# Optimization experiments

Measured on AMD Instinct MI355X. Metric: run time of the kernel, lower is better.

The kernel has to match this reference:

```python
import jax, jax.numpy as jnp
import numpy as np

HEAD_SIZE = 8
MODEL_SIZE = 512
K_SIZE = 64
V_SIZE = 64
B, L = 4, 2048


def setup_inputs() -> dict:
    key = jax.random.key(0)
    ks = jax.random.split(key, 12)
    s = 0.02
    inp = {
        "q": jax.random.normal(ks[0], (B, L, MODEL_SIZE), jnp.float32),
        "k": jax.random.normal(ks[1], (B, L, MODEL_SIZE), jnp.float32),
        "v": jax.random.normal(ks[2], (B, L, MODEL_SIZE), jnp.float32),
        "attn_mask": jax.random.randint(ks[3], (B, L, L), 0, 2).astype(jnp.bool_),
        "Wq": jax.random.normal(ks[4], (K_SIZE, MODEL_SIZE), jnp.float32) * s,
        "bq": jnp.zeros((K_SIZE,), jnp.float32),
        "Wk": jax.random.normal(ks[5], (K_SIZE, MODEL_SIZE), jnp.float32) * s,
        "bk": jnp.zeros((K_SIZE,), jnp.float32),
        "Wv": jax.random.normal(ks[6], (V_SIZE, MODEL_SIZE), jnp.float32) * s,
        "bv": jnp.zeros((V_SIZE,), jnp.float32),
        "Wp": jax.random.normal(ks[7], (MODEL_SIZE, HEAD_SIZE * V_SIZE), jnp.float32) * s,
        "bp": jnp.zeros((MODEL_SIZE,), jnp.float32),
    }
    return inp


def reference(q, k, v, attn_mask, Wq, bq, Wk, bk, Wv, bv, Wp, bp):
    # Original module applies the same linear_q/k/v to head-repeated tensors,
    # so every head is identical; compute once and tile (exactly equal math).
    temperature = jnp.asarray(MODEL_SIZE, q.dtype) ** 0.5  # note: sqrt(model_size), not sqrt(k_size)
    qp = jnp.einsum('bld,kd->blk', q, Wq) + bq  # (B, Lq, k_size)
    kp = jnp.einsum('bld,kd->blk', k, Wk) + bk  # (B, Lk, k_size)
    vp = jnp.einsum('bld,kd->blk', v, Wv) + bv  # (B, Lk, v_size)
    attn = jnp.einsum('bqd,bkd->bqk', qp, kp) / temperature  # (B, Lq, Lk)
    attn = jnp.where(attn_mask, -jnp.inf, attn)
    attn = jax.nn.softmax(attn, axis=-1)  # dropout is identity at eval
    out = jnp.einsum('bqk,bkd->bqd', attn, vp)  # (B, Lq, v_size)
    out = jnp.tile(out, (1, 1, HEAD_SIZE))  # concat of identical per-head outputs
    out = jnp.einsum('blh,mh->blm', out, Wp) + bp  # (B, Lq, model_size)
    return out
```

## Files before the change

kernel.cpp:

```cpp
#include <hip/hip_runtime.h>

#define B_ 4
#define L_ 2048
#define MD_ 512
#define KV_ 64
#define NKT_ (L_ / 64)
#define KSPLIT 16
#define NT_ 2

typedef unsigned short u16;
typedef unsigned char u8;
typedef unsigned int u32;
typedef unsigned long long u64;
typedef __attribute__((ext_vector_type(8))) short bf16x8;
typedef __attribute__((ext_vector_type(4))) float f32x4;
typedef __attribute__((ext_vector_type(4))) u32 u32x4;
typedef __attribute__((ext_vector_type(4))) u16 u16x4;

#define INV_T 0.044194173824159216f

static __device__ __forceinline__ u16 f2bf(float x) {
  u32 u = __float_as_uint(x);
  return (u16)((u + 0x7FFFu + ((u >> 16) & 1u)) >> 16);
}
static __device__ __forceinline__ float bf2f(u16 u) {
  return __uint_as_float((u32)u << 16);
}
static __device__ __forceinline__ f32x4 zero4() {
  f32x4 z = {0.f, 0.f, 0.f, 0.f};
  return z;
}
static __device__ __forceinline__ f32x4 mfma16(bf16x8 a, bf16x8 b, f32x4 c) {
  return __builtin_amdgcn_mfma_f32_16x16x32_bf16(a, b, c, 0, 0, 0);
}

__global__ __launch_bounds__(256) void mha_prep(
    const float* __restrict__ Wq, const float* __restrict__ Wk,
    const float* __restrict__ Wv, const float* __restrict__ bq,
    const float* __restrict__ bk, const float* __restrict__ bv,
    const float* __restrict__ Wp, u16* __restrict__ WtT,
    float* __restrict__ bqkv, u16* __restrict__ WpT) {
  int t = blockIdx.x * 256 + threadIdx.x;
  if (t < 3 * 64 * 512) {
    int p = t >> 15, c = (t >> 9) & 63, d = t & 511;
    const float* W = (p == 0) ? Wq : ((p == 1) ? Wk : Wv);
    WtT[(p * 64 + c) * 520 + d] = f2bf(W[c * 512 + d]);
  } else if (t < 3 * 64 * 512 + 512 * 64) {
    int i = t - 3 * 64 * 512;
    int m = i >> 6, d = i & 63;
    float s = 0.f;
#pragma unroll
    for (int h = 0; h < 8; h++) s += Wp[m * 512 + h * 64 + d];
    WpT[m * 72 + d] = f2bf(s);
  } else if (t < 3 * 64 * 512 + 512 * 64 + 192) {
    int j = t - (3 * 64 * 512 + 512 * 64);
    int p = j >> 6;
    const float* bb = (p == 0) ? bq : ((p == 1) ? bk : bv);
    bqkv[j] = bb[j & 63];
  }
}

__global__ __launch_bounds__(256) void mha_proj(
    const float* __restrict__ q, const float* __restrict__ k,
    const float* __restrict__ v, const u16* __restrict__ WtT,
    const float* __restrict__ bqkv, u16* __restrict__ qp,
    u16* __restrict__ kp, u16* __restrict__ vpt) {
  __shared__ __align__(16) u16 X[3][32][520];
  __shared__ __align__(16) u16 Xv[32][72];
  const int tid = threadIdx.x;
  const int r0 = blockIdx.x * 32;
#pragma unroll 4
  for (int i = 0; i < 48; i++) {
    int e = tid + i * 256;
    int p = e >> 12, r = (e >> 7) & 31, dq = (e & 127) << 2;
    const float* src = (p == 0) ? q : ((p == 1) ? k : v);
    f32x4 xv = *(const f32x4*)(src + (size_t)(r0 + r) * 512 + dq);
    u16x4 w4 = {f2bf(xv[0]), f2bf(xv[1]), f2bf(xv[2]), f2bf(xv[3])};
    *(u16x4*)&X[p][r][dq] = w4;
  }
  __syncthreads();
  const int w = tid >> 6, l = tid & 63, g = l >> 4, li = l & 15;
  const int mt = w & 1, half = w >> 1;
  f32x4 acc[6];
#pragma unroll
  for (int i = 0; i < 6; i++) acc[i] = zero4();

  if (half == 0) {
#pragma unroll 4
    for (int ks = 0; ks < 16; ks++) {
      const int ko = g * 8 + ks * 32;
      bf16x8 a0 = *(const bf16x8*)&X[0][mt * 16 + li][ko];
      bf16x8 a1 = *(const bf16x8*)&X[1][mt * 16 + li][ko];
      acc[0] = mfma16(a0, *(const bf16x8*)(WtT + (0 * 64 + 0 + li) * 520 + ko), acc[0]);
      acc[1] = mfma16(a0, *(const bf16x8*)(WtT + (0 * 64 + 16 + li) * 520 + ko), acc[1]);
      acc[2] = mfma16(a0, *(const bf16x8*)(WtT + (0 * 64 + 32 + li) * 520 + ko), acc[2]);
      acc[3] = mfma16(a0, *(const bf16x8*)(WtT + (0 * 64 + 48 + li) * 520 + ko), acc[3]);
      acc[4] = mfma16(a1, *(const bf16x8*)(WtT + (1 * 64 + 0 + li) * 520 + ko), acc[4]);
      acc[5] = mfma16(a1, *(const bf16x8*)(WtT + (1 * 64 + 16 + li) * 520 + ko), acc[5]);
    }
  } else {
#pragma unroll 4
    for (int ks = 0; ks < 16; ks++) {
      const int ko = g * 8 + ks * 32;
      bf16x8 a1 = *(const bf16x8*)&X[1][mt * 16 + li][ko];
      bf16x8 a2 = *(const bf16x8*)&X[2][mt * 16 + li][ko];
      acc[0] = mfma16(a1, *(const bf16x8*)(WtT + (1 * 64 + 32 + li) * 520 + ko), acc[0]);
      acc[1] = mfma16(a1, *(const bf16x8*)(WtT + (1 * 64 + 48 + li) * 520 + ko), acc[1]);
      acc[2] = mfma16(a2, *(const bf16x8*)(WtT + (2 * 64 + 0 + li) * 520 + ko), acc[2]);
      acc[3] = mfma16(a2, *(const bf16x8*)(WtT + (2 * 64 + 16 + li) * 520 + ko), acc[3]);
      acc[4] = mfma16(a2, *(const bf16x8*)(WtT + (2 * 64 + 32 + li) * 520 + ko), acc[4]);
      acc[5] = mfma16(a2, *(const bf16x8*)(WtT + (2 * 64 + 48 + li) * 520 + ko), acc[5]);
    }
  }
#pragma unroll
  for (int i = 0; i < 6; i++) {
    int nt = half * 6 + i;
    int p = nt >> 2, c4 = nt & 3;
    float bias = bqkv[nt * 16 + li];
#pragma unroll
    for (int j = 0; j < 4; j++) {
      int row = r0 + mt * 16 + g * 4 + j;
      u16 val = f2bf(acc[i][j] + bias);
      if (p == 0)
        qp[(size_t)row * 64 + c4 * 16 + li] = val;
      else if (p == 1)
        kp[(size_t)row * 64 + c4 * 16 + li] = val;
      else
        Xv[mt * 16 + g * 4 + j][c4 * 16 + li] = val;
    }
  }
  __syncthreads();
  {
    int d = tid >> 2, ch = tid & 3;
    size_t bb_ = (size_t)(r0 >> 11), kk = (size_t)(r0 & 2047);
    u16 tmp[8];
#pragma unroll
    for (int r = 0; r < 8; r++) tmp[r] = Xv[ch * 8 + r][d];
    *(bf16x8*)(vpt + (bb_ * 64 + d) * 2048 + kk + ch * 8) = *(bf16x8*)tmp;
  }
}

__global__ __launch_bounds__(256, 4) void mha_attn(
    const u16* __restrict__ qp, const u16* __restrict__ kp,
    const u16* __restrict__ vpt, const int* __restrict__ mask,
    u16* __restrict__ po, float* __restrict__ pl) {
  __shared__ __align__(16) char Klds[16384];
  __shared__ __align__(16) char Vlds[16384];
  __shared__ __align__(16) u16 Plds[4][16][72];
  __shared__ __align__(8) u64 Mb[64][2];
  const int tid = threadIdx.x;
  const int w = tid >> 6, l = tid & 63, g = l >> 4, li = l & 15;
  const int b = blockIdx.y;
  const int q0 = blockIdx.x * 64;
  const int s = blockIdx.z;
  const size_t brow = (size_t)b * L_;
  const int k0 = s * 128;

  const int par = l >> 5, lc = l & 31;
  const int sh = ((l >> 1) & 1) * 32 + (l & 1) * 16;

  u32x4 mreg[4];
#pragma unroll
  for (int c = 0; c < 4; c++) {
    int rr = (w * 8 + c) * 2 + par;
    mreg[c] = *(const u32x4*)(mask + (brow + q0 + rr) * (size_t)L_ + k0 + lc * 4);
  }
  u32x4 kst[4];
#pragma unroll
  for (int i = 0; i < 4; i++) {
    int e = i * 256 + tid;
    kst[i] = *(const u32x4*)(kp + (brow + k0 + (e >> 3)) * 64 + (e & 7) * 8);
  }
  bf16x8 qf0 = *(const bf16x8*)(qp + (brow + q0 + w * 16 + li) * 64 + g * 8);
  bf16x8 qf1 =
      *(const bf16x8*)(qp + (brow + q0 + w * 16 + li) * 64 + g * 8 + 32);
#pragma unroll
  for (int i = 0; i < 4; i++) {
    int e = i * 256 + tid;
    int r = e >> 3, c = (e & 7) * 16;
    *(u32x4*)(Klds + r * 128 + (c ^ ((r & 7) << 4))) = kst[i];
  }
#pragma unroll
  for (int c = 0; c < 4; c++) {
    u64 bal[4];
#pragma unroll
    for (int j = 0; j < 4; j++) bal[j] = __ballot(mreg[c][j] != 0);
    u64 pk = 0;
#pragma unroll
    for (int j = 0; j < 4; j++) pk |= ((bal[j] >> sh) & 0xFFFFull) << (16 * j);
    if (l < 4) Mb[(w * 8 + c) * 2 + (l >> 1)][l & 1] = pk;
  }
#pragma unroll
  for (int c = 0; c < 4; c++) {
    int rr = (w * 8 + 4 + c) * 2 + par;
    mreg[c] = *(const u32x4*)(mask + (brow + q0 + rr) * (size_t)L_ + k0 + lc * 4);
  }
  u32x4 vst[4];
#pragma unroll
  for (int i = 0; i < 4; i++) {
    int e = i * 256 + tid;
    vst[i] = *(const u32x4*)(vpt + ((size_t)b * 64 + (e >> 4)) * 2048 + k0 +
                             (e & 15) * 8);
  }
#pragma unroll
  for (int i = 0; i < 4; i++) {
    int e = i * 256 + tid;
    int d = e >> 4, c = (e & 15) * 16;
    *(u32x4*)(Vlds + d * 256 + (c ^ ((d & 7) << 4))) = vst[i];
  }
#pragma unroll
  for (int c = 0; c < 4; c++) {
    u64 bal[4];
#pragma unroll
    for (int j = 0; j < 4; j++) bal[j] = __ballot(mreg[c][j] != 0);
    u64 pk = 0;
#pragma unroll
    for (int j = 0; j < 4; j++) pk |= ((bal[j] >> sh) & 0xFFFFull) << (16 * j);
    if (l < 4) Mb[(w * 8 + 4 + c) * 2 + (l >> 1)][l & 1] = pk;
  }

  f32x4 o[4];
#pragma unroll
  for (int i = 0; i < 4; i++) o[i] = zero4();
  float rsl = 0.f;

  const int cA = (g * 16) ^ ((li & 7) << 4);
  const int cB = (g * 16 + 64) ^ ((li & 7) << 4);
  const int vx = (li & 7) << 4;

  __syncthreads();

#pragma unroll
  for (int kt = 0; kt < NT_; kt++) {
    const u64 pk = Mb[w * 16 + li][kt];
    f32x4 sacc[4];
#pragma unroll
    for (int nt = 0; nt < 4; nt++) {
      const int kr = kt * 64 + nt * 16 + li;
      bf16x8 kf0 = *(const bf16x8*)(Klds + kr * 128 + cA);
      bf16x8 kf1 = *(const bf16x8*)(Klds + kr * 128 + cB);
      sacc[nt] = mfma16(kf0, qf0, zero4());
      sacc[nt] = mfma16(kf1, qf1, sacc[nt]);
    }
#pragma unroll
    for (int nt = 0; nt < 4; nt++) {
      float pv[4];
#pragma unroll
      for (int r = 0; r < 4; r++) {
        float ex = __expf(sacc[nt][r] * INV_T);
        pv[r] = ((pk >> (r * 16 + nt * 4 + g)) & 1) ? 0.f : ex;
        rsl += pv[r];
      }
      u16x4 pkw = {f2bf(pv[0]), f2bf(pv[1]), f2bf(pv[2]), f2bf(pv[3])};
      *(u16x4*)&Plds[w][li][nt * 16 + 4 * g] = pkw;
    }
#pragma unroll
    for (int ks = 0; ks < 2; ks++) {
      bf16x8 pa = *(const bf16x8*)&Plds[w][li][ks * 32 + g * 8];
      const int vcol = (kt * 128 + ks * 64 + g * 16) ^ vx;
#pragma unroll
      for (int dt = 0; dt < 4; dt++) {
        bf16x8 vb = *(const bf16x8*)(Vlds + (dt * 16 + li) * 256 + vcol);
        o[dt] = mfma16(pa, vb, o[dt]);
      }
    }
  }
  rsl += __shfl_xor(rsl, 16);
  rsl += __shfl_xor(rsl, 32);
#pragma unroll
  for (int j = 0; j < 4; j++) {
    size_t r = brow + q0 + w * 16 + g * 4 + j;
    size_t base = (r * KSPLIT + s) * 64;
#pragma unroll
    for (int dt = 0; dt < 4; dt++) po[base + dt * 16 + li] = f2bf(o[dt][j]);
  }
  if (l < 16) pl[(brow + q0 + w * 16 + l) * KSPLIT + s] = rsl;
}

__global__ __launch_bounds__(128) void mha_fin(const u16* __restrict__ po,
                                               const float* __restrict__ pl,
                                               const u16* __restrict__ WpT,
                                               const float* __restrict__ bp,
                                               float* __restrict__ out) {
  __shared__ __align__(16) u16 A[32][72];
  const int tid = threadIdx.x;
  const size_t r0 = (size_t)blockIdx.x * 32;
  {
    const int rr = tid >> 2, dc = tid & 3;
    float accd[16];
#pragma unroll
    for (int j = 0; j < 16; j++) accd[j] = 0.f;
    float Lsum = 0.f;
#pragma unroll 4
    for (int i = 0; i < KSPLIT; i++) {
      const u16* p = po + ((r0 + rr) * KSPLIT + i) * 64 + dc * 16;
      u32x4 lo = *(const u32x4*)p;
      u32x4 hi = *(const u32x4*)(p + 8);
#pragma unroll
      for (int j = 0; j < 4; j++) {
        accd[2 * j + 0] += bf2f((u16)(lo[j] & 0xFFFF));
        accd[2 * j + 1] += bf2f((u16)(lo[j] >> 16));
        accd[8 + 2 * j + 0] += bf2f((u16)(hi[j] & 0xFFFF));
        accd[8 + 2 * j + 1] += bf2f((u16)(hi[j] >> 16));
      }
      Lsum += pl[(r0 + rr) * KSPLIT + i];
    }
    float inv = 1.f / Lsum;
#pragma unroll
    for (int j = 0; j < 16; j++) A[rr][dc * 16 + j] = f2bf(accd[j] * inv);
  }
  __syncthreads();
  const int w = tid >> 6, l = tid & 63, g = l >> 4, li = l & 15;
  bf16x8 a0 = *(const bf16x8*)&A[w * 16 + li][g * 8];
  bf16x8 a1 = *(const bf16x8*)&A[w * 16 + li][g * 8 + 32];
#pragma unroll 4
  for (int nt = 0; nt < 32; nt++) {
    bf16x8 b0 = *(const bf16x8*)(WpT + (nt * 16 + li) * 72 + g * 8);
    bf16x8 b1 = *(const bf16x8*)(WpT + (nt * 16 + li) * 72 + g * 8 + 32);
    f32x4 acc = zero4();
    acc = mfma16(a0, b0, acc);
    acc = mfma16(a1, b1, acc);
    float bias = bp[nt * 16 + li];
#pragma unroll
    for (int j = 0; j < 4; j++)
      out[(r0 + w * 16 + g * 4 + j) * 512 + nt * 16 + li] = acc[j] + bias;
  }
}

extern "C" void kernel_launch(void* const* d_in, const int* in_sizes, int n_in,
                              void* d_out, int out_size, void* d_ws,
                              size_t ws_size, hipStream_t stream) {
  const float* q = (const float*)d_in[0];
  const float* k = (const float*)d_in[1];
  const float* v = (const float*)d_in[2];
  const int* mask = (const int*)d_in[3];
  const float* Wq = (const float*)d_in[4];
  const float* bq = (const float*)d_in[5];
  const float* Wk = (const float*)d_in[6];
  const float* bk = (const float*)d_in[7];
  const float* Wv = (const float*)d_in[8];
  const float* bv = (const float*)d_in[9];
  const float* Wp = (const float*)d_in[10];
  const float* bp = (const float*)d_in[11];

  char* ws = (char*)d_ws;
  u16* qp = (u16*)(ws + 0);
  u16* kp = (u16*)(ws + 1048576);
  u16* vpt = (u16*)(ws + 2097152);
  u16* WtT = (u16*)(ws + 4194304);
  float* bqkv = (float*)(ws + 4393984);
  u16* WpT = (u16*)(ws + 4394752);
  u16* po = (u16*)(ws + 4468736);
  float* pl = (float*)(ws + 21245952);

  mha_prep<<<dim3(513), dim3(256), 0, stream>>>(Wq, Wk, Wv, bq, bk, bv, Wp,
                                                WtT, bqkv, WpT);
  mha_proj<<<dim3(256), dim3(256), 0, stream>>>(q, k, v, WtT, bqkv, qp, kp,
                                                vpt);
  mha_attn<<<dim3(32, 4, KSPLIT), dim3(256), 0, stream>>>(qp, kp, vpt, mask,
                                                          po, pl);
  mha_fin<<<dim3(256), dim3(128), 0, stream>>>(po, pl, WpT, bp,
                                               (float*)d_out);
}
```

Before: 59.94 us.

## Drop LDS staging in attention kernel, read K/V from global, halve KSPLIT

The attention kernel no longer stages K and V tiles through shared memory. Each wave now reads its K and V MFMA fragments straight from global memory (through the cache), and the mask is ballot-packed into per-lane registers instead of a shared bitmask table. KSPLIT drops from 16 to 8, so each block covers 256 keys in 4 tiles, which halves the partial outputs the finalize kernel must reduce, and the pl workspace offset moves to match. This removes the block-wide barrier and LDS traffic, at the cost of more redundant global/L2 reads across the four waves and fewer blocks in the grid.

```diff
diff --git a/kernel.cpp b/kernel.cpp
--- a/kernel.cpp
+++ b/kernel.cpp
@@ -4,9 +4,8 @@
 #define L_ 2048
 #define MD_ 512
 #define KV_ 64
-#define NKT_ (L_ / 64)
-#define KSPLIT 16
-#define NT_ 2
+#define KSPLIT 8
+#define TILES 4
 
 typedef unsigned short u16;
 typedef unsigned char u8;
@@ -144,123 +143,89 @@
     const u16* __restrict__ qp, const u16* __restrict__ kp,
     const u16* __restrict__ vpt, const int* __restrict__ mask,
     u16* __restrict__ po, float* __restrict__ pl) {
-  __shared__ __align__(16) char Klds[16384];
-  __shared__ __align__(16) char Vlds[16384];
   __shared__ __align__(16) u16 Plds[4][16][72];
-  __shared__ __align__(8) u64 Mb[64][2];
   const int tid = threadIdx.x;
   const int w = tid >> 6, l = tid & 63, g = l >> 4, li = l & 15;
   const int b = blockIdx.y;
   const int q0 = blockIdx.x * 64;
   const int s = blockIdx.z;
   const size_t brow = (size_t)b * L_;
-  const int k0 = s * 128;
-
-  const int par = l >> 5, lc = l & 31;
-  const int sh = ((l >> 1) & 1) * 32 + (l & 1) * 16;
-
-  u32x4 mreg[4];
-#pragma unroll
-  for (int c = 0; c < 4; c++) {
-    int rr = (w * 8 + c) * 2 + par;
-    mreg[c] = *(const u32x4*)(mask + (brow + q0 + rr) * (size_t)L_ + k0 + lc * 4);
-  }
-  u32x4 kst[4];
-#pragma unroll
-  for (int i = 0; i < 4; i++) {
-    int e = i * 256 + tid;
-    kst[i] = *(const u32x4*)(kp + (brow + k0 + (e >> 3)) * 64 + (e & 7) * 8);
-  }
+  const int k0 = s * 256;
+
+  u64 mb0 = 0, mb1 = 0, mb2 = 0, mb3 = 0;
+  const int* mbase = mask + (brow + q0 + w * 16) * (size_t)L_ + k0;
+#pragma unroll
+  for (int i = 0; i < 16; i += 8) {
+    u32x4 mr[8];
+#pragma unroll
+    for (int ii = 0; ii < 8; ii++)
+      mr[ii] = *(const u32x4*)(mbase + (size_t)(i + ii) * L_ + l * 4);
+#pragma unroll
+    for (int ii = 0; ii < 8; ii++) {
+      u64 b0 = __ballot(mr[ii][0] != 0);
+      u64 b1 = __ballot(mr[ii][1] != 0);
+      u64 b2 = __ballot(mr[ii][2] != 0);
+      u64 b3 = __ballot(mr[ii][3] != 0);
+      const bool sel = (li == i + ii);
+      mb0 = sel ? b0 : mb0;
+      mb1 = sel ? b1 : mb1;
+      mb2 = sel ? b2 : mb2;
+      mb3 = sel ? b3 : mb3;
+    }
+  }
+
   bf16x8 qf0 = *(const bf16x8*)(qp + (brow + q0 + w * 16 + li) * 64 + g * 8);
   bf16x8 qf1 =
       *(const bf16x8*)(qp + (brow + q0 + w * 16 + li) * 64 + g * 8 + 32);
-#pragma unroll
-  for (int i = 0; i < 4; i++) {
-    int e = i * 256 + tid;
-    int r = e >> 3, c = (e & 7) * 16;
-    *(u32x4*)(Klds + r * 128 + (c ^ ((r & 7) << 4))) = kst[i];
-  }
-#pragma unroll
-  for (int c = 0; c < 4; c++) {
-    u64 bal[4];
-#pragma unroll
-    for (int j = 0; j < 4; j++) bal[j] = __ballot(mreg[c][j] != 0);
-    u64 pk = 0;
-#pragma unroll
-    for (int j = 0; j < 4; j++) pk |= ((bal[j] >> sh) & 0xFFFFull) << (16 * j);
-    if (l < 4) Mb[(w * 8 + c) * 2 + (l >> 1)][l & 1] = pk;
-  }
-#pragma unroll
-  for (int c = 0; c < 4; c++) {
-    int rr = (w * 8 + 4 + c) * 2 + par;
-    mreg[c] = *(const u32x4*)(mask + (brow + q0 + rr) * (size_t)L_ + k0 + lc * 4);
-  }
-  u32x4 vst[4];
-#pragma unroll
-  for (int i = 0; i < 4; i++) {
-    int e = i * 256 + tid;
-    vst[i] = *(const u32x4*)(vpt + ((size_t)b * 64 + (e >> 4)) * 2048 + k0 +
-                             (e & 15) * 8);
-  }
-#pragma unroll
-  for (int i = 0; i < 4; i++) {
-    int e = i * 256 + tid;
-    int d = e >> 4, c = (e & 15) * 16;
-    *(u32x4*)(Vlds + d * 256 + (c ^ ((d & 7) << 4))) = vst[i];
-  }
-#pragma unroll
-  for (int c = 0; c < 4; c++) {
-    u64 bal[4];
-#pragma unroll
-    for (int j = 0; j < 4; j++) bal[j] = __ballot(mreg[c][j] != 0);
-    u64 pk = 0;
-#pragma unroll
-    for (int j = 0; j < 4; j++) pk |= ((bal[j] >> sh) & 0xFFFFull) << (16 * j);
-    if (l < 4) Mb[(w * 8 + 4 + c) * 2 + (l >> 1)][l & 1] = pk;
-  }
 
   f32x4 o[4];
 #pragma unroll
   for (int i = 0; i < 4; i++) o[i] = zero4();
   float rsl = 0.f;
 
-  const int cA = (g * 16) ^ ((li & 7) << 4);
-  const int cB = (g * 16 + 64) ^ ((li & 7) << 4);
-  const int vx = (li & 7) << 4;
-
-  __syncthreads();
-
-#pragma unroll
-  for (int kt = 0; kt < NT_; kt++) {
-    const u64 pk = Mb[w * 16 + li][kt];
+#pragma unroll
+  for (int t = 0; t < TILES; t++) {
+    const size_t kb = brow + k0 + t * 64;
     f32x4 sacc[4];
 #pragma unroll
     for (int nt = 0; nt < 4; nt++) {
-      const int kr = kt * 64 + nt * 16 + li;
-      bf16x8 kf0 = *(const bf16x8*)(Klds + kr * 128 + cA);
-      bf16x8 kf1 = *(const bf16x8*)(Klds + kr * 128 + cB);
+      bf16x8 kf0 = *(const bf16x8*)(kp + (kb + nt * 16 + li) * 64 + g * 8);
+      bf16x8 kf1 = *(const bf16x8*)(kp + (kb + nt * 16 + li) * 64 + g * 8 + 32);
       sacc[nt] = mfma16(kf0, qf0, zero4());
       sacc[nt] = mfma16(kf1, qf1, sacc[nt]);
     }
 #pragma unroll
     for (int nt = 0; nt < 4; nt++) {
-      float pv[4];
-#pragma unroll
-      for (int r = 0; r < 4; r++) {
-        float ex = __expf(sacc[nt][r] * INV_T);
-        pv[r] = ((pk >> (r * 16 + nt * 4 + g)) & 1) ? 0.f : ex;
-        rsl += pv[r];
-      }
-      u16x4 pkw = {f2bf(pv[0]), f2bf(pv[1]), f2bf(pv[2]), f2bf(pv[3])};
+      const int sh = t * 16 + nt * 4 + g;
+      float pv0, pv1, pv2, pv3;
+      {
+        float ex = __expf(sacc[nt][0] * INV_T);
+        pv0 = ((mb0 >> sh) & 1) ? 0.f : ex;
+      }
+      {
+        float ex = __expf(sacc[nt][1] * INV_T);
+        pv1 = ((mb1 >> sh) & 1) ? 0.f : ex;
+      }
+      {
+        float ex = __expf(sacc[nt][2] * INV_T);
+        pv2 = ((mb2 >> sh) & 1) ? 0.f : ex;
+      }
+      {
+        float ex = __expf(sacc[nt][3] * INV_T);
+        pv3 = ((mb3 >> sh) & 1) ? 0.f : ex;
+      }
+      rsl += pv0 + pv1 + pv2 + pv3;
+      u16x4 pkw = {f2bf(pv0), f2bf(pv1), f2bf(pv2), f2bf(pv3)};
       *(u16x4*)&Plds[w][li][nt * 16 + 4 * g] = pkw;
     }
 #pragma unroll
     for (int ks = 0; ks < 2; ks++) {
       bf16x8 pa = *(const bf16x8*)&Plds[w][li][ks * 32 + g * 8];
-      const int vcol = (kt * 128 + ks * 64 + g * 16) ^ vx;
 #pragma unroll
       for (int dt = 0; dt < 4; dt++) {
-        bf16x8 vb = *(const bf16x8*)(Vlds + (dt * 16 + li) * 256 + vcol);
+        bf16x8 vb =
+            *(const bf16x8*)(vpt + ((size_t)b * 64 + dt * 16 + li) * 2048 +
+                             k0 + t * 64 + ks * 32 + g * 8);
         o[dt] = mfma16(pa, vb, o[dt]);
       }
     }
@@ -351,7 +316,7 @@
   float* bqkv = (float*)(ws + 4393984);
   u16* WpT = (u16*)(ws + 4394752);
   u16* po = (u16*)(ws + 4468736);
-  float* pl = (float*)(ws + 21245952);
+  float* pl = (float*)(ws + 12857344);
 
   mha_prep<<<dim3(513), dim3(256), 0, stream>>>(Wq, Wk, Wv, bq, bk, bv, Wp,
                                                 WtT, bqkv, WpT);
```

Result: slower. 79.24 us (+32.2%).

## Stage mask via direct global-to-LDS loads and hold V fragments in registers

Applied to the files above, without the earlier changes.

The attention kernel now copies the int mask tile straight into LDS with global_load_lds and packs it into per-lane bitmasks with wave ballots after one barrier. It drops the register-staged mask ballot-packing and the V LDS tile, loading V fragments from global memory directly into registers, with the second half prefetched during the first tile's QK compute. The 32KB int mask buffer raises LDS use, so launch bounds drop from 4 to 2 blocks per CU, trading occupancy for fewer LDS round trips and less packing work. Mask bit indexing changes to match the new ballot layout.

```diff
diff --git a/kernel.cpp b/kernel.cpp
--- a/kernel.cpp
+++ b/kernel.cpp
@@ -4,9 +4,8 @@
 #define L_ 2048
 #define MD_ 512
 #define KV_ 64
-#define NKT_ (L_ / 64)
 #define KSPLIT 16
-#define NT_ 2
+#define TILES 2
 
 typedef unsigned short u16;
 typedef unsigned char u8;
@@ -140,14 +139,13 @@
   }
 }
 
-__global__ __launch_bounds__(256, 4) void mha_attn(
+__global__ __launch_bounds__(256, 2) void mha_attn(
     const u16* __restrict__ qp, const u16* __restrict__ kp,
     const u16* __restrict__ vpt, const int* __restrict__ mask,
     u16* __restrict__ po, float* __restrict__ pl) {
+  __shared__ __align__(16) int Mint[64 * 128];
   __shared__ __align__(16) char Klds[16384];
-  __shared__ __align__(16) char Vlds[16384];
   __shared__ __align__(16) u16 Plds[4][16][72];
-  __shared__ __align__(8) u64 Mb[64][2];
   const int tid = threadIdx.x;
   const int w = tid >> 6, l = tid & 63, g = l >> 4, li = l & 15;
   const int b = blockIdx.y;
@@ -156,83 +154,61 @@
   const size_t brow = (size_t)b * L_;
   const int k0 = s * 128;
 
-  const int par = l >> 5, lc = l & 31;
-  const int sh = ((l >> 1) & 1) * 32 + (l & 1) * 16;
-
-  u32x4 mreg[4];
-#pragma unroll
-  for (int c = 0; c < 4; c++) {
-    int rr = (w * 8 + c) * 2 + par;
-    mreg[c] = *(const u32x4*)(mask + (brow + q0 + rr) * (size_t)L_ + k0 + lc * 4);
-  }
+#pragma unroll
+  for (int i = 0; i < 8; i++) {
+    int CI = i * 256 + tid;
+    const int* gsrc =
+        mask + (brow + q0 + (CI >> 5)) * (size_t)L_ + k0 + (CI & 31) * 4;
+    __builtin_amdgcn_global_load_lds(gsrc, &Mint[CI * 4], 16, 0, 0);
+  }
+
+  bf16x8 qf0 = *(const bf16x8*)(qp + (brow + q0 + w * 16 + li) * 64 + g * 8);
+  bf16x8 qf1 =
+      *(const bf16x8*)(qp + (brow + q0 + w * 16 + li) * 64 + g * 8 + 32);
+  bf16x8 vf0[8], vf1[8];
+#pragma unroll
+  for (int ks = 0; ks < 2; ks++)
+#pragma unroll
+    for (int dt = 0; dt < 4; dt++)
+      vf0[ks * 4 + dt] =
+          *(const bf16x8*)(vpt + ((size_t)b * 64 + dt * 16 + li) * 2048 + k0 +
+                           0 * 64 + ks * 32 + g * 8);
   u32x4 kst[4];
 #pragma unroll
   for (int i = 0; i < 4; i++) {
     int e = i * 256 + tid;
     kst[i] = *(const u32x4*)(kp + (brow + k0 + (e >> 3)) * 64 + (e & 7) * 8);
   }
-  bf16x8 qf0 = *(const bf16x8*)(qp + (brow + q0 + w * 16 + li) * 64 + g * 8);
-  bf16x8 qf1 =
-      *(const bf16x8*)(qp + (brow + q0 + w * 16 + li) * 64 + g * 8 + 32);
 #pragma unroll
   for (int i = 0; i < 4; i++) {
     int e = i * 256 + tid;
     int r = e >> 3, c = (e & 7) * 16;
     *(u32x4*)(Klds + r * 128 + (c ^ ((r & 7) << 4))) = kst[i];
   }
-#pragma unroll
-  for (int c = 0; c < 4; c++) {
-    u64 bal[4];
-#pragma unroll
-    for (int j = 0; j < 4; j++) bal[j] = __ballot(mreg[c][j] != 0);
-    u64 pk = 0;
-#pragma unroll
-    for (int j = 0; j < 4; j++) pk |= ((bal[j] >> sh) & 0xFFFFull) << (16 * j);
-    if (l < 4) Mb[(w * 8 + c) * 2 + (l >> 1)][l & 1] = pk;
-  }
-#pragma unroll
-  for (int c = 0; c < 4; c++) {
-    int rr = (w * 8 + 4 + c) * 2 + par;
-    mreg[c] = *(const u32x4*)(mask + (brow + q0 + rr) * (size_t)L_ + k0 + lc * 4);
-  }
-  u32x4 vst[4];
-#pragma unroll
-  for (int i = 0; i < 4; i++) {
-    int e = i * 256 + tid;
-    vst[i] = *(const u32x4*)(vpt + ((size_t)b * 64 + (e >> 4)) * 2048 + k0 +
-                             (e & 15) * 8);
-  }
-#pragma unroll
-  for (int i = 0; i < 4; i++) {
-    int e = i * 256 + tid;
-    int d = e >> 4, c = (e & 15) * 16;
-    *(u32x4*)(Vlds + d * 256 + (c ^ ((d & 7) << 4))) = vst[i];
-  }
-#pragma unroll
-  for (int c = 0; c < 4; c++) {
-    u64 bal[4];
-#pragma unroll
-    for (int j = 0; j < 4; j++) bal[j] = __ballot(mreg[c][j] != 0);
-    u64 pk = 0;
-#pragma unroll
-    for (int j = 0; j < 4; j++) pk |= ((bal[j] >> sh) & 0xFFFFull) << (16 * j);
-    if (l < 4) Mb[(w * 8 + 4 + c) * 2 + (l >> 1)][l & 1] = pk;
+
+  __syncthreads();
+
+  u64 mblo = 0, mbhi = 0;
+#pragma unroll
+  for (int rr = 0; rr < 16; rr++) {
+    const int R = w * 16 + rr;
+    u64 blo = __ballot(Mint[R * 128 + l] != 0);
+    u64 bhi = __ballot(Mint[R * 128 + 64 + l] != 0);
+    const bool sel = (li == rr);
+    mblo = sel ? blo : mblo;
+    mbhi = sel ? bhi : mbhi;
   }
 
   f32x4 o[4];
 #pragma unroll
   for (int i = 0; i < 4; i++) o[i] = zero4();
   float rsl = 0.f;
-
   const int cA = (g * 16) ^ ((li & 7) << 4);
   const int cB = (g * 16 + 64) ^ ((li & 7) << 4);
-  const int vx = (li & 7) << 4;
-
-  __syncthreads();
-
-#pragma unroll
-  for (int kt = 0; kt < NT_; kt++) {
-    const u64 pk = Mb[w * 16 + li][kt];
+
+#pragma unroll
+  for (int kt = 0; kt < TILES; kt++) {
+    const u64 mb = (kt == 0) ? mblo : mbhi;
     f32x4 sacc[4];
 #pragma unroll
     for (int nt = 0; nt < 4; nt++) {
@@ -242,13 +218,22 @@
       sacc[nt] = mfma16(kf0, qf0, zero4());
       sacc[nt] = mfma16(kf1, qf1, sacc[nt]);
     }
+    if (kt == 0) {
+#pragma unroll
+      for (int ks = 0; ks < 2; ks++)
+#pragma unroll
+        for (int dt = 0; dt < 4; dt++)
+          vf1[ks * 4 + dt] =
+              *(const bf16x8*)(vpt + ((size_t)b * 64 + dt * 16 + li) * 2048 +
+                               k0 + 64 + ks * 32 + g * 8);
+    }
 #pragma unroll
     for (int nt = 0; nt < 4; nt++) {
       float pv[4];
 #pragma unroll
       for (int r = 0; r < 4; r++) {
         float ex = __expf(sacc[nt][r] * INV_T);
-        pv[r] = ((pk >> (r * 16 + nt * 4 + g)) & 1) ? 0.f : ex;
+        pv[r] = ((mb >> (nt * 16 + 4 * g + r)) & 1) ? 0.f : ex;
         rsl += pv[r];
       }
       u16x4 pkw = {f2bf(pv[0]), f2bf(pv[1]), f2bf(pv[2]), f2bf(pv[3])};
@@ -257,10 +242,9 @@
 #pragma unroll
     for (int ks = 0; ks < 2; ks++) {
       bf16x8 pa = *(const bf16x8*)&Plds[w][li][ks * 32 + g * 8];
-      const int vcol = (kt * 128 + ks * 64 + g * 16) ^ vx;
 #pragma unroll
       for (int dt = 0; dt < 4; dt++) {
-        bf16x8 vb = *(const bf16x8*)(Vlds + (dt * 16 + li) * 256 + vcol);
+        bf16x8 vb = (kt == 0) ? vf0[ks * 4 + dt] : vf1[ks * 4 + dt];
         o[dt] = mfma16(pa, vb, o[dt]);
       }
     }
```

New measurement: 71.58 us. 1.19x slower.
